# Kernel tuning notes

Measured on AMD Instinct MI355X. Metric: run time of the kernel, lower is better.

## Reference

```python
import jax, jax.numpy as jnp
import numpy as np

EPS = 1e-12  # F.normalize clamp_min eps


def setup_inputs() -> dict:
    key = jax.random.key(0)
    k1, k2, k3, k4 = jax.random.split(key, 4)
    E, A, D, S = 1000000, 100000, 128, 1024
    return {
        "edge_weights": jax.random.uniform(k1, (E,), dtype=jnp.float32),
        "s_indices": jax.random.randint(k2, (E,), 0, S, dtype=jnp.int32),
        "a_indices": jax.random.randint(k3, (E,), 0, A, dtype=jnp.int32),
        "agent_features": jax.random.normal(k4, (A, D), dtype=jnp.float32),
        "num_s": S,
    }


def reference(edge_weights, s_indices, a_indices, agent_features, num_s):
    # Per-edge gathered agent features: [E, D]
    feats_e = agent_features[a_indices]
    ones = jnp.ones_like(edge_weights)
    counts = jax.ops.segment_sum(ones, s_indices, num_segments=num_s)  # [S]
    safe_counts = jnp.maximum(counts, 1.0)

    # Per-source mean feature: [S, D]
    sum_feats = jax.ops.segment_sum(feats_e, s_indices, num_segments=num_s)
    mean_feats = sum_feats / safe_counts[:, None]

    # L2-normalize (eps-clamped norm, matching F.normalize)
    feats_norm = feats_e / jnp.maximum(
        jnp.linalg.norm(feats_e, axis=1, keepdims=True), EPS)
    mean_norm = mean_feats / jnp.maximum(
        jnp.linalg.norm(mean_feats, axis=1, keepdims=True), EPS)

    # Cosine similarity of each edge's agent features to its source mean: [E]
    sims = jnp.sum(feats_norm * mean_norm[s_indices], axis=1)

    # Per-source mean weight, per-edge variance, similarity-weighted variance
    mean_w = jax.ops.segment_sum(edge_weights, s_indices, num_segments=num_s) / safe_counts
    var = (edge_weights - mean_w[s_indices]) ** 2
    wv = sims * var

    # Per-source mean of weighted variance; sources with <=1 edge contribute 0
    seg_mean_wv = jax.ops.segment_sum(wv, s_indices, num_segments=num_s) / safe_counts
    valid = counts > 1.0
    total = jnp.sum(jnp.where(valid, seg_mean_wv, 0.0))
    return total / num_s
```

## Files before the change

kernel.cpp:

```cpp
#include <hip/hip_runtime.h>
#include <math.h>

#define EPS 1e-12f

static constexpr int S_FIXED = 1024;
static constexpr int D_DIM   = 128;
static constexpr int NBLK    = 256;
static constexpr int P_SPLIT = 2;
static constexpr float INVW  = 1.0f / 32767.0f;

typedef float floatx2 __attribute__((ext_vector_type(2)));

#if defined(__has_builtin)
#if __has_builtin(__builtin_amdgcn_cvt_pk_fp8_f32) && __has_builtin(__builtin_amdgcn_cvt_pk_f32_fp8)
#define USE_HW_FP8 1
#endif
#endif

template <bool HI>
static __device__ __forceinline__ unsigned enc_pair(float a, float b, unsigned old) {
#ifdef USE_HW_FP8
    return (unsigned)__builtin_amdgcn_cvt_pk_fp8_f32(a, b, (int)old, HI);
#else
    auto enc1 = [](float x) -> unsigned {
        unsigned u   = __float_as_uint(x);
        unsigned s   = (u >> 24) & 0x80u;
        unsigned mag = u & 0x7fffffffu;
        unsigned byte;
        if (mag >= 0x3C800000u) {
            unsigned rb = mag + 0x7ffffu + ((mag >> 20) & 1u);
            byte = s | (((rb >> 20) - 960u) & 0x7fu);
        } else {
            float t = __uint_as_float(mag) * 512.0f;
            unsigned m = (unsigned)(int)rintf(t);
            byte = s | m;
        }
        return byte;
    };
    unsigned v = enc1(a) | (enc1(b) << 8);
    return HI ? ((old & 0x0000ffffu) | (v << 16)) : ((old & 0xffff0000u) | v);
#endif
}

template <bool HI>
static __device__ __forceinline__ floatx2 dec_pair(unsigned v) {
#ifdef USE_HW_FP8
    return __builtin_amdgcn_cvt_pk_f32_fp8(v, HI);
#else
    auto dec1 = [](unsigned b) -> float {
        unsigned t = (b & 0x7fu) << 20;
        float a = __uint_as_float(t + 0x3C800000u);
        float r = (t < (1u << 23)) ? (a - 0.015625f) : (0.5f * a);
        return (b & 0x80u) ? -r : r;
    };
    unsigned h = HI ? (v >> 16) : (v & 0xffffu);
    floatx2 o;
    o.x = dec1(h & 0xffu);
    o.y = dec1((h >> 8) & 0xffu);
    return o;
#endif
}

__global__ __launch_bounds__(256) void normhist_kernel(const float* __restrict__ feats,
                                                       unsigned char* __restrict__ g8,
                                                       float* __restrict__ r_tab, int A,
                                                       const int* __restrict__ s_idx,
                                                       int* __restrict__ counts2d,
                                                       int E, int chunk, int ncb,
                                                       float* __restrict__ out) {
    if (blockIdx.x == 0 && threadIdx.x == 0) out[0] = 0.0f;
    if (blockIdx.x < (unsigned)ncb) {
        const int row = blockIdx.x * 16 + (threadIdx.x >> 4);
        const int sl  = threadIdx.x & 15;
        if (row >= A) return;
        const float4* fp = reinterpret_cast<const float4*>(feats + (size_t)row * D_DIM + sl * 8);
        const float4 v0 = fp[0], v1 = fp[1];
        float ss = v0.x*v0.x + v0.y*v0.y + v0.z*v0.z + v0.w*v0.w
                 + v1.x*v1.x + v1.y*v1.y + v1.z*v1.z + v1.w*v1.w;
#pragma unroll
        for (int o = 1; o < 16; o <<= 1) ss += __shfl_xor(ss, o);
        const float nrm = sqrtf(ss);
        const float inv = 1.0f / fmaxf(nrm, EPS);
        unsigned lo = enc_pair<false>(v0.x*inv, v0.y*inv, 0u);
        lo = enc_pair<true>(v0.z*inv, v0.w*inv, lo);
        unsigned hi = enc_pair<false>(v1.x*inv, v1.y*inv, 0u);
        hi = enc_pair<true>(v1.z*inv, v1.w*inv, hi);
        *reinterpret_cast<uint2*>(g8 + (size_t)row * D_DIM + sl * 8) = make_uint2(lo, hi);
        if (sl == 0) r_tab[row] = nrm;
    } else {
        __shared__ int h[S_FIXED];
        for (int i = threadIdx.x; i < S_FIXED; i += 256) h[i] = 0;
        __syncthreads();
        const int b  = blockIdx.x - ncb;
        const int lo = b * chunk;
        const int hi = min(E, lo + chunk);
        for (int i = lo + threadIdx.x; i < hi; i += 256)
            atomicAdd(&h[s_idx[i]], 1);
        __syncthreads();
        for (int i = threadIdx.x; i < S_FIXED; i += 256)
            counts2d[b * S_FIXED + i] = h[i];
    }
}

__global__ __launch_bounds__(256) void scan_blocks_kernel(int* __restrict__ counts2d,
                                                          int* __restrict__ counts) {
    const int wv = threadIdx.x >> 6, lane = threadIdx.x & 63;
    const int bin = blockIdx.x * 4 + wv;
    int running = 0;
#pragma unroll
    for (int b0 = 0; b0 < NBLK; b0 += 64) {
        const int idx = (b0 + lane) * S_FIXED + bin;
        const int c = counts2d[idx];
        int inc = c;
#pragma unroll
        for (int o = 1; o < 64; o <<= 1) {
            int t = __shfl_up(inc, o);
            if (lane >= o) inc += t;
        }
        counts2d[idx] = running + inc - c;
        running += __shfl(inc, 63);
    }
    if (lane == 0) counts[bin] = running;
}

__global__ __launch_bounds__(256) void scatter3_kernel(const int* __restrict__ s_idx,
                                                       const int* __restrict__ a_idx,
                                                       const float* __restrict__ w,
                                                       const int* __restrict__ counts2d,
                                                       const int* __restrict__ counts,
                                                       int* __restrict__ binstart_g,
                                                       unsigned* __restrict__ bin4,
                                                       int E, int chunk) {
    __shared__ int cur[S_FIXED];
    __shared__ int tsum[256];
    const int b = blockIdx.x;
    const int t = threadIdx.x;

    int c[4]; int sum = 0;
#pragma unroll
    for (int i = 0; i < 4; ++i) { c[i] = counts[t * 4 + i]; sum += c[i]; }
    tsum[t] = sum;
    __syncthreads();
    for (int off = 1; off < 256; off <<= 1) {
        int v = (t >= off) ? tsum[t - off] : 0;
        __syncthreads();
        tsum[t] += v;
        __syncthreads();
    }
    int base = tsum[t] - sum;
#pragma unroll
    for (int i = 0; i < 4; ++i) {
        const int bi = t * 4 + i;
        cur[bi] = base + counts2d[b * S_FIXED + bi];
        if (b == 0) binstart_g[bi] = base;
        base += c[i];
    }
    __syncthreads();

    const int lo = b * chunk;
    const int hi = min(E, lo + chunk);
    for (int i = lo + threadIdx.x; i < hi; i += 256) {
        const int s   = s_idx[i];
        const int pos = atomicAdd(&cur[s], 1);
        const unsigned w15 = (unsigned)(int)rintf(w[i] * 32767.0f);
        bin4[pos] = (unsigned)a_idx[i] | (w15 << 17);
    }
}

__global__ __launch_bounds__(256) void partial_kernel(
    const unsigned char* __restrict__ g8,
    const float*         __restrict__ r_tab,
    const int*           __restrict__ counts,
    const int*           __restrict__ binstart,
    const unsigned*      __restrict__ bin4,
    float*               __restrict__ part,
    float*               __restrict__ partW,
    int A)
{
    const int s     = blockIdx.x >> 1;
    const int p     = blockIdx.x & 1;
    const int cnt   = counts[s];
    const int start = binstart[s];
    const int end   = start + cnt;
    const int wave  = threadIdx.x >> 6;
    const int lane  = threadIdx.x & 63;
    const int egrp  = lane >> 5;
    const int sl    = lane & 31;

    __shared__ unsigned smem[4 * 2048];
    __shared__ float redW[4];
    unsigned* wrow = smem + wave * 2048;
    const int rdbase = egrp * 32 + sl;

    floatx2 acc[4][2];
#pragma unroll
    for (int v = 0; v < 4; ++v)
#pragma unroll
        for (int q = 0; q < 2; ++q) acc[v][q] = (floatx2)(0.0f);
    float accW = 0.0f;

    for (int base = start + (p * 4 + wave) * 64; base < end; base += P_SPLIT * 256) {
        const int rem = min(64, end - base);
        const unsigned rec = bin4[base + lane];
        if (lane < rem) accW += (float)(rec >> 17) * INVW;

        asm volatile("s_waitcnt lgkmcnt(0)" ::: "memory");
        __builtin_amdgcn_sched_barrier(0);

#pragma unroll
        for (int j = 0; j < 32; ++j) {
            const unsigned r0 = (unsigned)__builtin_amdgcn_readlane((int)rec, 2 * j);
            const unsigned r1 = (unsigned)__builtin_amdgcn_readlane((int)rec, 2 * j + 1);
            const unsigned re = egrp ? r1 : r0;
            const int aj = min((int)(re & 0x1FFFFu), A - 1);
            const unsigned char* gp = g8 + (size_t)aj * D_DIM + sl * 4;
            __builtin_amdgcn_global_load_lds(
                (const __attribute__((address_space(1))) void*)gp,
                (__attribute__((address_space(3))) void*)(wrow + j * 64),
                4, 0, 0);
        }
        asm volatile("s_waitcnt vmcnt(0)" ::: "memory");
        __builtin_amdgcn_sched_barrier(0);

#pragma unroll
        for (int j = 0; j < 32; ++j) {
            const unsigned gu = wrow[rdbase + j * 64];
            const unsigned q0 = (unsigned)__builtin_amdgcn_readlane((int)rec, 2 * j);
            const unsigned q1 = (unsigned)__builtin_amdgcn_readlane((int)rec, 2 * j + 1);
            const unsigned re = egrp ? q1 : q0;
            const int   e    = 2 * j + egrp;
            const float mask = (e < rem) ? 1.0f : 0.0f;
            const float wj   = (float)(re >> 17) * INVW * mask;
            floatx2 f[2];
            f[0] = dec_pair<false>(gu);
            f[1] = dec_pair<true>(gu);
            const floatx2 cu  = (floatx2)(mask);
            const floatx2 cw  = (floatx2)(wj);
            const floatx2 cw2 = (floatx2)(wj * wj);
#pragma unroll
            for (int q = 0; q < 2; ++q) {
                acc[1][q] = __builtin_elementwise_fma(cu,  f[q], acc[1][q]);
                acc[2][q] = __builtin_elementwise_fma(cw,  f[q], acc[2][q]);
                acc[3][q] = __builtin_elementwise_fma(cw2, f[q], acc[3][q]);
            }
            const int a_e = min((int)(re & 0x1FFFFu), A - 1);
            const float rr = r_tab[a_e] * mask;
            const floatx2 cr = (floatx2)(rr);
#pragma unroll
            for (int q = 0; q < 2; ++q)
                acc[0][q] = __builtin_elementwise_fma(cr, f[q], acc[0][q]);
        }
    }

#pragma unroll
    for (int v = 0; v < 4; ++v)
#pragma unroll
        for (int q = 0; q < 2; ++q) {
            acc[v][q].x += __shfl_xor(acc[v][q].x, 32);
            acc[v][q].y += __shfl_xor(acc[v][q].y, 32);
        }
#pragma unroll
    for (int o = 32; o > 0; o >>= 1) accW += __shfl_xor(accW, o);

    float* redf = reinterpret_cast<float*>(wrow);
    if (lane < 32) {
#pragma unroll
        for (int v = 0; v < 4; ++v)
#pragma unroll
            for (int q = 0; q < 2; ++q) {
                redf[v * D_DIM + sl * 4 + 2 * q]     = acc[v][q].x;
                redf[v * D_DIM + sl * 4 + 2 * q + 1] = acc[v][q].y;
            }
    }
    if (lane == 0) redW[wave] = accW;
    __syncthreads();

    float* po = part + (size_t)(s * P_SPLIT + p) * (4 * D_DIM);
    const float* r0f = reinterpret_cast<const float*>(smem);
    for (int i = threadIdx.x; i < 4 * D_DIM; i += 256)
        po[i] = r0f[i] + r0f[2048 + i] + r0f[4096 + i] + r0f[6144 + i];
    if (threadIdx.x == 0)
        partW[s * P_SPLIT + p] = redW[0] + redW[1] + redW[2] + redW[3];
}

__global__ __launch_bounds__(1024) void finish_kernel(
    const float* __restrict__ part,
    const float* __restrict__ partW,
    const int*   __restrict__ counts,
    const int*   __restrict__ num_s_ptr,
    float*       __restrict__ out)
{
    const int wv   = threadIdx.x >> 6;
    const int lane = threadIdx.x & 63;
    const int s    = blockIdx.x * 16 + wv;

    float2 V[4];
#pragma unroll
    for (int v = 0; v < 4; ++v) V[v] = make_float2(0.f, 0.f);
    float sumW = 0.0f;
#pragma unroll
    for (int p = 0; p < P_SPLIT; ++p) {
#pragma unroll
        for (int v = 0; v < 4; ++v) {
            const float2 x = *reinterpret_cast<const float2*>(
                part + ((size_t)s * P_SPLIT + p) * (4 * D_DIM) + v * D_DIM + lane * 2);
            V[v].x += x.x; V[v].y += x.y;
        }
        if (lane == 0) sumW += partW[s * P_SPLIT + p];
    }
    const int   cnt      = counts[s];
    const float safe     = (float)max(cnt, 1);
    const float inv_safe = 1.0f / safe;

    const float mx = V[0].x * inv_safe, my = V[0].y * inv_safe;
    float ss = mx * mx + my * my;
    float s0 = V[1].x * mx + V[1].y * my;
    float s1 = V[2].x * mx + V[2].y * my;
    float s2 = V[3].x * mx + V[3].y * my;
#pragma unroll
    for (int o = 32; o > 0; o >>= 1) {
        ss += __shfl_xor(ss, o);
        s0 += __shfl_xor(s0, o);
        s1 += __shfl_xor(s1, o);
        s2 += __shfl_xor(s2, o);
    }

    __shared__ float bl[16];
    if (lane == 0) {
        float contrib = 0.0f;
        if (cnt > 1) {
            const float mw = sumW * inv_safe;
            const float mn = fmaxf(sqrtf(ss), EPS);
            contrib = (s2 - 2.0f * mw * s1 + mw * mw * s0) / mn * inv_safe
                      / (float)(*num_s_ptr);
        }
        bl[wv] = contrib;
    }
    __syncthreads();
    if (threadIdx.x == 0) {
        float t = 0.0f;
#pragma unroll
        for (int i = 0; i < 16; ++i) t += bl[i];
        atomicAdd(out, t);
    }
}

extern "C" void kernel_launch(void* const* d_in, const int* in_sizes, int n_in,
                              void* d_out, int out_size, void* d_ws, size_t ws_size,
                              hipStream_t stream) {
    const float* edge_w  = (const float*)d_in[0];
    const int*   s_idx   = (const int*)d_in[1];
    const int*   a_idx   = (const int*)d_in[2];
    const float* feats   = (const float*)d_in[3];
    const int*   num_s_p = (const int*)d_in[4];

    const int E = in_sizes[0];
    const int A = in_sizes[3] / D_DIM;

    float* out = (float*)d_out;

    char* p = (char*)d_ws;
    unsigned*      bin4     = (unsigned*)p;      p += (size_t)E * 4;
    int*           counts2d = (int*)p;           p += (size_t)NBLK * S_FIXED * 4;
    int*           binstart = (int*)p;           p += S_FIXED * 4;
    int*           counts   = (int*)p;           p += S_FIXED * 4;
    float*         partW    = (float*)p;         p += S_FIXED * P_SPLIT * 4;
    float*         part     = (float*)p;         p += (size_t)S_FIXED * P_SPLIT * 4 * D_DIM * 4;
    float*         r_tab    = (float*)p;         p += (size_t)A * 4;
    unsigned char* g8       = (unsigned char*)p; p += (size_t)A * D_DIM;

    const int chunk = (E + NBLK - 1) / NBLK;
    const int ncb   = (A + 15) / 16;

    normhist_kernel<<<ncb + NBLK, 256, 0, stream>>>(feats, g8, r_tab, A,
                                                    s_idx, counts2d, E, chunk, ncb, out);
    scan_blocks_kernel<<<S_FIXED / 4, 256, 0, stream>>>(counts2d, counts);
    scatter3_kernel<<<NBLK, 256, 0, stream>>>(s_idx, a_idx, edge_w, counts2d, counts,
                                              binstart, bin4, E, chunk);
    partial_kernel<<<S_FIXED * P_SPLIT, 256, 0, stream>>>(g8, r_tab, counts, binstart,
                                                          bin4, part, partW, A);
    finish_kernel<<<S_FIXED / 16, 1024, 0, stream>>>(part, partW, counts, num_s_p, out);
}
```

Measured before the change: 91.68 us.

## Fuse partial and finish kernels, drop LDS-staged gathers for direct loads

Merges the per-source partial accumulation and the finish reduction into one kernel with one block per source, which removes the P_SPLIT split, the global partial buffers and one kernel launch. The fp8 feature gather now uses direct per-lane global loads inside a lambda instead of global_load_lds staging with explicit waitcnt barriers. The per-edge records are reloaded from global memory rather than broadcast by readlane. The cost is half as many blocks (1024 rather than 2048), which may reduce latency hiding for the random gathers, and per-source atomicAdd on the output.

```diff
diff --git a/kernel.cpp b/kernel.cpp
--- a/kernel.cpp
+++ b/kernel.cpp
@@ -6,7 +6,6 @@
 static constexpr int S_FIXED = 1024;
 static constexpr int D_DIM   = 128;
 static constexpr int NBLK    = 256;
-static constexpr int P_SPLIT = 2;
 static constexpr float INVW  = 1.0f / 32767.0f;
 
 typedef float floatx2 __attribute__((ext_vector_type(2)));
@@ -167,18 +166,17 @@
     }
 }
 
-__global__ __launch_bounds__(256) void partial_kernel(
+__global__ __launch_bounds__(256) void partial_finish_kernel(
     const unsigned char* __restrict__ g8,
     const float*         __restrict__ r_tab,
     const int*           __restrict__ counts,
     const int*           __restrict__ binstart,
     const unsigned*      __restrict__ bin4,
-    float*               __restrict__ part,
-    float*               __restrict__ partW,
+    const int*           __restrict__ num_s_ptr,
+    float*               __restrict__ out,
     int A)
 {
-    const int s     = blockIdx.x >> 1;
-    const int p     = blockIdx.x & 1;
+    const int s     = blockIdx.x;
     const int cnt   = counts[s];
     const int start = binstart[s];
     const int end   = start + cnt;
@@ -187,11 +185,6 @@
     const int egrp  = lane >> 5;
     const int sl    = lane & 31;
 
-    __shared__ unsigned smem[4 * 2048];
-    __shared__ float redW[4];
-    unsigned* wrow = smem + wave * 2048;
-    const int rdbase = egrp * 32 + sl;
-
     floatx2 acc[4][2];
 #pragma unroll
     for (int v = 0; v < 4; ++v)
@@ -199,56 +192,45 @@
         for (int q = 0; q < 2; ++q) acc[v][q] = (floatx2)(0.0f);
     float accW = 0.0f;
 
-    for (int base = start + (p * 4 + wave) * 64; base < end; base += P_SPLIT * 256) {
+    auto body = [&](unsigned rec, float mask) {
+        int aj = (int)(rec & 0x1FFFFu);
+        aj = min(aj, A - 1);
+        const float wj = (float)(rec >> 17) * INVW * mask;
+        const float rj = r_tab[aj] * mask;
+        const unsigned gu = *reinterpret_cast<const unsigned*>(g8 + (size_t)aj * D_DIM + sl * 4);
+        floatx2 f[2];
+        f[0] = dec_pair<false>(gu);
+        f[1] = dec_pair<true>(gu);
+        const floatx2 cr  = (floatx2)(rj);
+        const floatx2 cu  = (floatx2)(mask);
+        const floatx2 cw  = (floatx2)(wj);
+        const floatx2 cw2 = (floatx2)(wj * wj);
+#pragma unroll
+        for (int q = 0; q < 2; ++q) {
+            acc[0][q] = __builtin_elementwise_fma(cr,  f[q], acc[0][q]);
+            acc[1][q] = __builtin_elementwise_fma(cu,  f[q], acc[1][q]);
+            acc[2][q] = __builtin_elementwise_fma(cw,  f[q], acc[2][q]);
+            acc[3][q] = __builtin_elementwise_fma(cw2, f[q], acc[3][q]);
+        }
+    };
+
+    for (int base = start + wave * 64; base < end; base += 256) {
         const int rem = min(64, end - base);
-        const unsigned rec = bin4[base + lane];
-        if (lane < rem) accW += (float)(rec >> 17) * INVW;
-
-        asm volatile("s_waitcnt lgkmcnt(0)" ::: "memory");
-        __builtin_amdgcn_sched_barrier(0);
-
-#pragma unroll
-        for (int j = 0; j < 32; ++j) {
-            const unsigned r0 = (unsigned)__builtin_amdgcn_readlane((int)rec, 2 * j);
-            const unsigned r1 = (unsigned)__builtin_amdgcn_readlane((int)rec, 2 * j + 1);
-            const unsigned re = egrp ? r1 : r0;
-            const int aj = min((int)(re & 0x1FFFFu), A - 1);
-            const unsigned char* gp = g8 + (size_t)aj * D_DIM + sl * 4;
-            __builtin_amdgcn_global_load_lds(
-                (const __attribute__((address_space(1))) void*)gp,
-                (__attribute__((address_space(3))) void*)(wrow + j * 64),
-                4, 0, 0);
-        }
-        asm volatile("s_waitcnt vmcnt(0)" ::: "memory");
-        __builtin_amdgcn_sched_barrier(0);
-
-#pragma unroll
-        for (int j = 0; j < 32; ++j) {
-            const unsigned gu = wrow[rdbase + j * 64];
-            const unsigned q0 = (unsigned)__builtin_amdgcn_readlane((int)rec, 2 * j);
-            const unsigned q1 = (unsigned)__builtin_amdgcn_readlane((int)rec, 2 * j + 1);
-            const unsigned re = egrp ? q1 : q0;
-            const int   e    = 2 * j + egrp;
-            const float mask = (e < rem) ? 1.0f : 0.0f;
-            const float wj   = (float)(re >> 17) * INVW * mask;
-            floatx2 f[2];
-            f[0] = dec_pair<false>(gu);
-            f[1] = dec_pair<true>(gu);
-            const floatx2 cu  = (floatx2)(mask);
-            const floatx2 cw  = (floatx2)(wj);
-            const floatx2 cw2 = (floatx2)(wj * wj);
-#pragma unroll
-            for (int q = 0; q < 2; ++q) {
-                acc[1][q] = __builtin_elementwise_fma(cu,  f[q], acc[1][q]);
-                acc[2][q] = __builtin_elementwise_fma(cw,  f[q], acc[2][q]);
-                acc[3][q] = __builtin_elementwise_fma(cw2, f[q], acc[3][q]);
+        if (lane < rem)
+            accW += (float)(bin4[base + lane] >> 17) * INVW;
+
+        if (rem == 64) {
+#pragma unroll
+            for (int j = 0; j < 32; ++j)
+                body(bin4[base + 2 * j + egrp], 1.0f);
+        } else {
+            const int jfull = rem >> 1;
+            for (int j = 0; j < jfull; ++j)
+                body(bin4[base + 2 * j + egrp], 1.0f);
+            if (rem & 1) {
+                const int e = (rem & ~1) + egrp;
+                body(bin4[base + e], (e < rem) ? 1.0f : 0.0f);
             }
-            const int a_e = min((int)(re & 0x1FFFFu), A - 1);
-            const float rr = r_tab[a_e] * mask;
-            const floatx2 cr = (floatx2)(rr);
-#pragma unroll
-            for (int q = 0; q < 2; ++q)
-                acc[0][q] = __builtin_elementwise_fma(cr, f[q], acc[0][q]);
         }
     }
 
@@ -262,86 +244,51 @@
 #pragma unroll
     for (int o = 32; o > 0; o >>= 1) accW += __shfl_xor(accW, o);
 
-    float* redf = reinterpret_cast<float*>(wrow);
+    __shared__ float red[4][4 * D_DIM];
+    __shared__ float redW[4];
     if (lane < 32) {
 #pragma unroll
         for (int v = 0; v < 4; ++v)
 #pragma unroll
             for (int q = 0; q < 2; ++q) {
-                redf[v * D_DIM + sl * 4 + 2 * q]     = acc[v][q].x;
-                redf[v * D_DIM + sl * 4 + 2 * q + 1] = acc[v][q].y;
+                red[wave][v * D_DIM + sl * 4 + 2 * q]     = acc[v][q].x;
+                red[wave][v * D_DIM + sl * 4 + 2 * q + 1] = acc[v][q].y;
             }
     }
     if (lane == 0) redW[wave] = accW;
     __syncthreads();
 
-    float* po = part + (size_t)(s * P_SPLIT + p) * (4 * D_DIM);
-    const float* r0f = reinterpret_cast<const float*>(smem);
-    for (int i = threadIdx.x; i < 4 * D_DIM; i += 256)
-        po[i] = r0f[i] + r0f[2048 + i] + r0f[4096 + i] + r0f[6144 + i];
-    if (threadIdx.x == 0)
-        partW[s * P_SPLIT + p] = redW[0] + redW[1] + redW[2] + redW[3];
-}
-
-__global__ __launch_bounds__(1024) void finish_kernel(
-    const float* __restrict__ part,
-    const float* __restrict__ partW,
-    const int*   __restrict__ counts,
-    const int*   __restrict__ num_s_ptr,
-    float*       __restrict__ out)
-{
-    const int wv   = threadIdx.x >> 6;
-    const int lane = threadIdx.x & 63;
-    const int s    = blockIdx.x * 16 + wv;
-
-    float2 V[4];
-#pragma unroll
-    for (int v = 0; v < 4; ++v) V[v] = make_float2(0.f, 0.f);
-    float sumW = 0.0f;
-#pragma unroll
-    for (int p = 0; p < P_SPLIT; ++p) {
+    if (wave == 0) {
+        float2 V[4];
 #pragma unroll
         for (int v = 0; v < 4; ++v) {
-            const float2 x = *reinterpret_cast<const float2*>(
-                part + ((size_t)s * P_SPLIT + p) * (4 * D_DIM) + v * D_DIM + lane * 2);
-            V[v].x += x.x; V[v].y += x.y;
-        }
-        if (lane == 0) sumW += partW[s * P_SPLIT + p];
-    }
-    const int   cnt      = counts[s];
-    const float safe     = (float)max(cnt, 1);
-    const float inv_safe = 1.0f / safe;
-
-    const float mx = V[0].x * inv_safe, my = V[0].y * inv_safe;
-    float ss = mx * mx + my * my;
-    float s0 = V[1].x * mx + V[1].y * my;
-    float s1 = V[2].x * mx + V[2].y * my;
-    float s2 = V[3].x * mx + V[3].y * my;
-#pragma unroll
-    for (int o = 32; o > 0; o >>= 1) {
-        ss += __shfl_xor(ss, o);
-        s0 += __shfl_xor(s0, o);
-        s1 += __shfl_xor(s1, o);
-        s2 += __shfl_xor(s2, o);
-    }
-
-    __shared__ float bl[16];
-    if (lane == 0) {
-        float contrib = 0.0f;
-        if (cnt > 1) {
-            const float mw = sumW * inv_safe;
-            const float mn = fmaxf(sqrtf(ss), EPS);
-            contrib = (s2 - 2.0f * mw * s1 + mw * mw * s0) / mn * inv_safe
-                      / (float)(*num_s_ptr);
-        }
-        bl[wv] = contrib;
-    }
-    __syncthreads();
-    if (threadIdx.x == 0) {
-        float t = 0.0f;
-#pragma unroll
-        for (int i = 0; i < 16; ++i) t += bl[i];
-        atomicAdd(out, t);
+            const int d = v * D_DIM + lane * 2;
+            V[v] = make_float2(red[0][d]     + red[1][d]     + red[2][d]     + red[3][d],
+                               red[0][d + 1] + red[1][d + 1] + red[2][d + 1] + red[3][d + 1]);
+        }
+        const float safe     = (float)max(cnt, 1);
+        const float inv_safe = 1.0f / safe;
+
+        const float mx = V[0].x * inv_safe, my = V[0].y * inv_safe;
+        float ss = mx * mx + my * my;
+        float s0 = V[1].x * mx + V[1].y * my;
+        float s1 = V[2].x * mx + V[2].y * my;
+        float s2 = V[3].x * mx + V[3].y * my;
+#pragma unroll
+        for (int o = 32; o > 0; o >>= 1) {
+            ss += __shfl_xor(ss, o);
+            s0 += __shfl_xor(s0, o);
+            s1 += __shfl_xor(s1, o);
+            s2 += __shfl_xor(s2, o);
+        }
+        if (lane == 0 && cnt > 1) {
+            const float sumW = redW[0] + redW[1] + redW[2] + redW[3];
+            const float mw   = sumW * inv_safe;
+            const float mn   = fmaxf(sqrtf(ss), EPS);
+            const float contrib = (s2 - 2.0f * mw * s1 + mw * mw * s0) / mn * inv_safe
+                                  / (float)(*num_s_ptr);
+            atomicAdd(out, contrib);
+        }
     }
 }
 
@@ -364,8 +311,6 @@
     int*           counts2d = (int*)p;           p += (size_t)NBLK * S_FIXED * 4;
     int*           binstart = (int*)p;           p += S_FIXED * 4;
     int*           counts   = (int*)p;           p += S_FIXED * 4;
-    float*         partW    = (float*)p;         p += S_FIXED * P_SPLIT * 4;
-    float*         part     = (float*)p;         p += (size_t)S_FIXED * P_SPLIT * 4 * D_DIM * 4;
     float*         r_tab    = (float*)p;         p += (size_t)A * 4;
     unsigned char* g8       = (unsigned char*)p; p += (size_t)A * D_DIM;
 
@@ -377,7 +322,6 @@
     scan_blocks_kernel<<<S_FIXED / 4, 256, 0, stream>>>(counts2d, counts);
     scatter3_kernel<<<NBLK, 256, 0, stream>>>(s_idx, a_idx, edge_w, counts2d, counts,
                                               binstart, bin4, E, chunk);
-    partial_kernel<<<S_FIXED * P_SPLIT, 256, 0, stream>>>(g8, r_tab, counts, binstart,
-                                                          bin4, part, partW, A);
-    finish_kernel<<<S_FIXED / 16, 1024, 0, stream>>>(part, partW, counts, num_s_p, out);
-}
+    partial_finish_kernel<<<S_FIXED, 256, 0, stream>>>(g8, r_tab, counts, binstart,
+                                                       bin4, num_s_p, out, A);
+}
```

New measurement: 79.36 us. 1.16x faster.
